# Kernel tuning notes

Hardware: AMD Instinct MI355X
Metric: run time of the kernel (lower is better)

The kernel has to match this reference:

```python
import jax, jax.numpy as jnp
import numpy as np

N_QUBITS = 12
RANK = 1024
K = 4            # outcomes per qubit
D = 2 ** N_QUBITS
N_IDX = 1_000_000


def setup_inputs() -> dict:
    key = jax.random.key(0)
    k1, k2, k3, k4 = jax.random.split(key, 4)
    params = jax.random.normal(k1, (2, D, RANK), dtype=jnp.float32)
    M_real = jax.random.normal(k2, (K, 2, 2), dtype=jnp.float32)
    M_imag = jax.random.normal(k3, (K, 2, 2), dtype=jnp.float32)
    P_idxs = jax.random.randint(k4, (N_IDX,), 0, K ** N_QUBITS, dtype=jnp.int64)
    return {"params": params, "M_real": M_real, "M_imag": M_imag, "P_idxs": P_idxs}


def _qmt(rho, M, n_qubits):
    """Born rule: P[s1..sN] = Tr[(M_{s1} x ... x M_{sN}) rho].
    Sequential per-qubit contraction; T has shape [K^n, 2^(N-n), 2^(N-n)]."""
    T = rho[None, :, :]  # axes: (done outcomes, row legs j, col legs i)
    for _ in range(n_qubits):
        k, r, c = T.shape[0], T.shape[1] // 2, T.shape[2] // 2
        Tt = T.reshape(k, 2, r, 2, c)  # (k, j_n, j_rest, i_n, i_rest)
        # Tr contribution: sum_{i,j} M[s,i,j] * rho[j,i]
        T = jnp.einsum('sij,kjait->ksat', M, Tt).reshape(k * M.shape[0], r, c)
    return T.reshape(-1)  # [K^N] complex


def reference(params, M_real, M_imag, P_idxs):
    # rho = U U^H / Tr(U U^H)
    U = jax.lax.complex(params[0], params[1])            # [D, RANK] complex64
    rho = U @ U.conj().T                                  # [D, D]
    rho = rho / jnp.trace(rho)
    M = jax.lax.complex(M_real, M_imag)                   # [K, 2, 2] complex64
    P_all = _qmt(rho, M, N_QUBITS).real                   # [K^N] float32
    return P_all[P_idxs]
```

## Files before the change

kernel.cpp:

```cpp
#include <hip/hip_runtime.h>

#define D 4096
#define RANK 1024
#define K2 2048
#define UELEMS 4194304ULL
#define NTOT 16777216ULL
#define QSCALE 16000.0f

typedef __attribute__((ext_vector_type(4))) int i32x4;

__device__ float g_inv_tr[1];
__device__ float g_scale[D];
__device__ float g_mdre[16];
__device__ float g_mdim[16];

static __device__ __forceinline__ void load_lds16(const void* g, void* l) {
    __builtin_amdgcn_global_load_lds(
        (const __attribute__((address_space(1))) unsigned int*)g,
        (__attribute__((address_space(3))) unsigned int*)l, 16, 0, 0);
}

__global__ __launch_bounds__(256) void convert_w_i8(const float* __restrict__ P,
                                                    const float* __restrict__ Mre,
                                                    const float* __restrict__ Mim,
                                                    char* __restrict__ Wh,
                                                    char* __restrict__ Wl,
                                                    char* __restrict__ N2h,
                                                    char* __restrict__ N2l)
{
    if (blockIdx.x == 0 && threadIdx.x < 16) {
        const int s = threadIdx.x >> 2, i = (threadIdx.x >> 1) & 1, j = threadIdx.x & 1;
        g_mdre[threadIdx.x] =  Mre[s * 4 + j * 2 + i];
        g_mdim[threadIdx.x] = -Mim[s * 4 + j * 2 + i];
    }

    const int w = threadIdx.x >> 6, lane = threadIdx.x & 63;
    const int row = blockIdx.x * 4 + w;

    float ur[16], ui[16];
    const float* pr = P + (size_t)row * RANK + lane * 16;
    const float* pi = P + UELEMS + (size_t)row * RANK + lane * 16;
    #pragma unroll
    for (int q = 0; q < 4; ++q) {
        const float4 a = ((const float4*)pr)[q];
        const float4 b = ((const float4*)pi)[q];
        ur[q * 4 + 0] = a.x; ur[q * 4 + 1] = a.y; ur[q * 4 + 2] = a.z; ur[q * 4 + 3] = a.w;
        ui[q * 4 + 0] = b.x; ui[q * 4 + 1] = b.y; ui[q * 4 + 2] = b.z; ui[q * 4 + 3] = b.w;
    }
    float mx = 0.f;
    #pragma unroll
    for (int e = 0; e < 16; ++e)
        mx = fmaxf(mx, fmaxf(fabsf(ur[e]), fabsf(ui[e])));
    #pragma unroll
    for (int off = 1; off < 64; off <<= 1)
        mx = fmaxf(mx, __shfl_xor(mx, off));
    const float inv = mx > 0.f ? QSCALE / mx : 0.f;
    if (lane == 0) g_scale[row] = mx / QSCALE;

    int hr[16], lr[16], hi[16], li[16];
    #pragma unroll
    for (int e = 0; e < 16; ++e) {
        float q = ur[e] * inv;
        float hf = rintf(q * 0.0078125f);
        hr[e] = (int)hf; lr[e] = (int)rintf(q - 128.f * hf);
        q = ui[e] * inv;
        hf = rintf(q * 0.0078125f);
        hi[e] = (int)hf; li[e] = (int)rintf(q - 128.f * hf);
    }
    uint4 phr, plr, phi, pli, pnh, pnl;
    unsigned* dst[6] = {(unsigned*)&phr, (unsigned*)&plr, (unsigned*)&phi,
                        (unsigned*)&pli, (unsigned*)&pnh, (unsigned*)&pnl};
    #pragma unroll
    for (int q = 0; q < 4; ++q) {
        unsigned a = 0, b = 0, c = 0, d = 0, e = 0, f = 0;
        #pragma unroll
        for (int k = 0; k < 4; ++k) {
            const int sh = k * 8;
            a |= (unsigned)(hr[q * 4 + k] & 255) << sh;
            b |= (unsigned)(lr[q * 4 + k] & 255) << sh;
            c |= (unsigned)(hi[q * 4 + k] & 255) << sh;
            d |= (unsigned)(li[q * 4 + k] & 255) << sh;
            e |= (unsigned)((-hi[q * 4 + k]) & 255) << sh;
            f |= (unsigned)((-li[q * 4 + k]) & 255) << sh;
        }
        dst[0][q] = a; dst[1][q] = b; dst[2][q] = c; dst[3][q] = d; dst[4][q] = e; dst[5][q] = f;
    }
    const size_t b1 = (size_t)row * 2048 + lane * 16;
    *(uint4*)&Wh[b1] = phr;          *(uint4*)&Wl[b1] = plr;
    *(uint4*)&Wh[b1 + 1024] = phi;   *(uint4*)&Wl[b1 + 1024] = pli;
    const size_t b2 = (size_t)row * 1024 + lane * 16;
    *(uint4*)&N2h[b2] = pnh;         *(uint4*)&N2l[b2] = pnl;
}

__global__ __launch_bounds__(256, 2) void gemm_rho_i8(const char* __restrict__ Wh,
                                                      const char* __restrict__ Wl,
                                                      const char* __restrict__ N2h,
                                                      const char* __restrict__ N2l,
                                                      float2* __restrict__ rho)
{
    __shared__ __align__(16) char sA1h[64 * 64];
    __shared__ __align__(16) char sA1l[64 * 64];
    __shared__ __align__(16) char sA2h[64 * 64];
    __shared__ __align__(16) char sA2l[64 * 64];
    __shared__ __align__(16) char sB1h[128 * 64];
    __shared__ __align__(16) char sB1l[128 * 64];
    __shared__ __align__(16) char sB2h[128 * 64];
    __shared__ __align__(16) char sB2l[128 * 64];
    __shared__ __align__(16) char sN2h[128 * 64];
    __shared__ __align__(16) char sN2l[128 * 64];

    const int b = blockIdx.x;
    int bj = (int)((65.0f - sqrtf(4225.0f - 4.0f * (float)b)) * 0.5f);
    while (bj > 0 && bj * (65 - bj) > b) --bj;
    while ((bj + 1) * (64 - bj) <= b) ++bj;
    const int bi = 2 * bj + (b - bj * (65 - bj));
    const int row0 = bi << 6, col0 = bj << 7;
    const bool full = (bi >= 2 * bj + 2);

    const int t = threadIdx.x;
    const int lane = t & 63, w = t >> 6;
    const int wr = w >> 1, wc = w & 1;

    const int rowA = t >> 2;
    const int kcA = (t & 3) ^ ((rowA >> 1) & 3);
    const size_t aoff = (size_t)(row0 + rowA) * 2048 + kcA * 16;
    const int ldsA = t * 16;
    size_t boff[2], boffN[2]; int ldsB[2];
    #pragma unroll
    for (int q = 0; q < 2; ++q) {
        const int g = q * 256 + t;
        const int rowB = g >> 2;
        const int kcB = (g & 3) ^ ((rowB >> 1) & 3);
        boff[q]  = (size_t)(col0 + rowB) * 2048 + kcB * 16;
        boffN[q] = (size_t)(col0 + rowB) * 1024 + kcB * 16;
        ldsB[q] = g * 16;
    }

    const int m = lane & 15, gq = lane >> 4;
    const int fko = (gq ^ ((m >> 1) & 3)) * 16;

    i32x4 rehh[2][4], remx[2][4], imhh[2][4], immx[2][4];
    #pragma unroll
    for (int i = 0; i < 2; ++i)
        #pragma unroll
        for (int j = 0; j < 4; ++j) {
            rehh[i][j] = (i32x4){0, 0, 0, 0}; remx[i][j] = (i32x4){0, 0, 0, 0};
            imhh[i][j] = (i32x4){0, 0, 0, 0}; immx[i][j] = (i32x4){0, 0, 0, 0};
        }

    for (int kt = 0; kt < RANK; kt += 64) {
        load_lds16(Wh + aoff + kt,        &sA1h[ldsA]);
        load_lds16(Wl + aoff + kt,        &sA1l[ldsA]);
        load_lds16(Wh + aoff + kt + 1024, &sA2h[ldsA]);
        load_lds16(Wl + aoff + kt + 1024, &sA2l[ldsA]);
        #pragma unroll
        for (int q = 0; q < 2; ++q) {
            load_lds16(Wh + boff[q] + kt,        &sB1h[ldsB[q]]);
            load_lds16(Wl + boff[q] + kt,        &sB1l[ldsB[q]]);
            load_lds16(Wh + boff[q] + kt + 1024, &sB2h[ldsB[q]]);
            load_lds16(Wl + boff[q] + kt + 1024, &sB2l[ldsB[q]]);
            load_lds16(N2h + boffN[q] + kt,      &sN2h[ldsB[q]]);
            load_lds16(N2l + boffN[q] + kt,      &sN2l[ldsB[q]]);
        }
        __syncthreads();

        i32x4 fa1h[2], fa1l[2], fa2h[2], fa2l[2];
        #pragma unroll
        for (int i = 0; i < 2; ++i) {
            const int off = (wr * 32 + i * 16 + m) * 64 + fko;
            fa1h[i] = *(const i32x4*)&sA1h[off];
            fa1l[i] = *(const i32x4*)&sA1l[off];
            fa2h[i] = *(const i32x4*)&sA2h[off];
            fa2l[i] = *(const i32x4*)&sA2l[off];
        }
        #pragma unroll
        for (int j = 0; j < 4; ++j) {
            const int off = (wc * 64 + j * 16 + m) * 64 + fko;
            const i32x4 b1h = *(const i32x4*)&sB1h[off];
            const i32x4 b1l = *(const i32x4*)&sB1l[off];
            const i32x4 b2h = *(const i32x4*)&sB2h[off];
            const i32x4 b2l = *(const i32x4*)&sB2l[off];
            const i32x4 n2h = *(const i32x4*)&sN2h[off];
            const i32x4 n2l = *(const i32x4*)&sN2l[off];
            #pragma unroll
            for (int i = 0; i < 2; ++i) {
                i32x4 r = rehh[i][j];
                r = __builtin_amdgcn_mfma_i32_16x16x64_i8(fa1h[i], b1h, r, 0, 0, 0);
                r = __builtin_amdgcn_mfma_i32_16x16x64_i8(fa2h[i], b2h, r, 0, 0, 0);
                rehh[i][j] = r;
                r = remx[i][j];
                r = __builtin_amdgcn_mfma_i32_16x16x64_i8(fa1h[i], b1l, r, 0, 0, 0);
                r = __builtin_amdgcn_mfma_i32_16x16x64_i8(fa1l[i], b1h, r, 0, 0, 0);
                r = __builtin_amdgcn_mfma_i32_16x16x64_i8(fa2h[i], b2l, r, 0, 0, 0);
                r = __builtin_amdgcn_mfma_i32_16x16x64_i8(fa2l[i], b2h, r, 0, 0, 0);
                remx[i][j] = r;
                r = imhh[i][j];
                r = __builtin_amdgcn_mfma_i32_16x16x64_i8(fa2h[i], b1h, r, 0, 0, 0);
                r = __builtin_amdgcn_mfma_i32_16x16x64_i8(fa1h[i], n2h, r, 0, 0, 0);
                imhh[i][j] = r;
                r = immx[i][j];
                r = __builtin_amdgcn_mfma_i32_16x16x64_i8(fa2h[i], b1l, r, 0, 0, 0);
                r = __builtin_amdgcn_mfma_i32_16x16x64_i8(fa2l[i], b1h, r, 0, 0, 0);
                r = __builtin_amdgcn_mfma_i32_16x16x64_i8(fa1h[i], n2l, r, 0, 0, 0);
                r = __builtin_amdgcn_mfma_i32_16x16x64_i8(fa1l[i], n2h, r, 0, 0, 0);
                immx[i][j] = r;
            }
        }
        __syncthreads();
    }

    #pragma unroll
    for (int i = 0; i < 2; ++i)
        #pragma unroll
        for (int j = 0; j < 4; ++j) {
            const int col = col0 + wc * 64 + j * 16 + m;
            const float sc = g_scale[col];
            #pragma unroll
            for (int r = 0; r < 4; ++r) {
                const int row = row0 + wr * 32 + i * 16 + gq * 4 + r;
                const float s2 = g_scale[row] * sc;
                const float re = s2 * (16384.f * (float)rehh[i][j][r] + 128.f * (float)remx[i][j][r]);
                const float im = s2 * (16384.f * (float)imhh[i][j][r] + 128.f * (float)immx[i][j][r]);
                if (full || row >= col) rho[(size_t)row * D + col] = make_float2(re, im);
                if (row > col && ((row >> 6) == (col >> 6)))
                    rho[(size_t)col * D + row] = make_float2(re, -im);
            }
        }
}

__global__ void trace_inv(const float2* __restrict__ rho)
{
    __shared__ float red[256];
    float s = 0.f;
    for (int d = threadIdx.x; d < D; d += 256)
        s += rho[(size_t)d * (D + 1)].x;
    red[threadIdx.x] = s;
    __syncthreads();
    for (int off = 128; off > 0; off >>= 1) {
        if (threadIdx.x < off) red[threadIdx.x] += red[threadIdx.x + off];
        __syncthreads();
    }
    if (threadIdx.x == 0) g_inv_tr[0] = 1.0f / red[0];
}

static __device__ __forceinline__ void qmt2(float2* x,
                                            const float* __restrict__ Mre,
                                            const float* __restrict__ Mim)
{
    float2 y[16];
    #pragma unroll
    for (int sb = 0; sb < 4; ++sb)
        #pragma unroll
        for (int ja = 0; ja < 2; ++ja)
            #pragma unroll
            for (int ia = 0; ia < 2; ++ia) {
                float2 acc = make_float2(0.f, 0.f);
                #pragma unroll
                for (int ib = 0; ib < 2; ++ib)
                    #pragma unroll
                    for (int jb = 0; jb < 2; ++jb) {
                        const float mr = Mre[sb * 4 + ib * 2 + jb];
                        const float mi = Mim[sb * 4 + ib * 2 + jb];
                        const float2 v = x[(ja * 2 + jb) * 4 + ia * 2 + ib];
                        acc.x += mr * v.x - mi * v.y;
                        acc.y += mr * v.y + mi * v.x;
                    }
                y[sb * 4 + ja * 2 + ia] = acc;
            }
    #pragma unroll
    for (int sa = 0; sa < 4; ++sa)
        #pragma unroll
        for (int sb = 0; sb < 4; ++sb) {
            float2 acc = make_float2(0.f, 0.f);
            #pragma unroll
            for (int ia = 0; ia < 2; ++ia)
                #pragma unroll
                for (int ja = 0; ja < 2; ++ja) {
                    const float mr = Mre[sa * 4 + ia * 2 + ja];
                    const float mi = Mim[sa * 4 + ia * 2 + ja];
                    const float2 v = y[sb * 4 + ja * 2 + ia];
                    acc.x += mr * v.x - mi * v.y;
                    acc.y += mr * v.y + mi * v.x;
                }
            x[sa * 4 + sb] = acc;
        }
}

static __device__ __forceinline__ void pA_pipeline(float2* x, float2* X, const int t,
                                                   const float* __restrict__ mre,
                                                   const float* __restrict__ mim)
{
    qmt2(x, mre, mim);
    #pragma unroll
    for (int d = 0; d < 16; ++d) X[t * 17 + d] = x[d];
    __syncthreads();
    const int a2 = t >> 6, t2 = (t >> 4) & 3, d1 = t & 15;
    #pragma unroll
    for (int j2 = 0; j2 < 4; ++j2)
        #pragma unroll
        for (int i2 = 0; i2 < 4; ++i2)
            x[j2 * 4 + i2] = X[((a2 * 4 + j2) * 16 + t2 * 4 + i2) * 17 + d1];
    __syncthreads();
    qmt2(x, mre, mim);
    #pragma unroll
    for (int d = 0; d < 16; ++d) X[(a2 * 4 + t2) * 257 + d * 16 + d1] = x[d];
    __syncthreads();
    const int e2 = t >> 4, e1 = t & 15;
    #pragma unroll
    for (int j2 = 0; j2 < 4; ++j2)
        #pragma unroll
        for (int i2 = 0; i2 < 4; ++i2)
            x[j2 * 4 + i2] = X[(j2 * 4 + i2) * 257 + e2 * 16 + e1];
    qmt2(x, mre, mim);
}

__global__ __launch_bounds__(256) void qmt_pAh(const float2* __restrict__ in,
                                               float2* __restrict__ out,
                                               const float* __restrict__ Mre,
                                               const float* __restrict__ Mim)
{
    __shared__ __align__(16) float2 X[256 * 17];
    const int t = threadIdx.x;
    const int g = blockIdx.x;
    int rr = (int)((sqrtf(8.f * (float)g + 1.f) - 1.f) * 0.5f);
    while (rr * (rr + 1) / 2 > g) --rr;
    while ((rr + 1) * (rr + 2) / 2 <= g) ++rr;
    const int cc = g - rr * (rr + 1) / 2;

    const int a4 = t >> 4, t4 = t & 15;
    float2 x0[16], x[16];
    #pragma unroll
    for (int j2 = 0; j2 < 4; ++j2) {
        const float2* p = in + ((size_t)(rr * 64 + a4 * 4 + j2)) * 4096 + cc * 64 + t4 * 4;
        const float4 v0 = ((const float4*)p)[0];
        const float4 v1 = ((const float4*)p)[1];
        x0[j2 * 4 + 0] = make_float2(v0.x, v0.y);
        x0[j2 * 4 + 1] = make_float2(v0.z, v0.w);
        x0[j2 * 4 + 2] = make_float2(v1.x, v1.y);
        x0[j2 * 4 + 3] = make_float2(v1.z, v1.w);
    }

    #pragma unroll
    for (int q = 0; q < 16; ++q) x[q] = x0[q];
    pA_pipeline(x, X, t, Mre, Mim);
    const int e2 = t >> 4, e1 = t & 15;
    const size_t ob0 = (size_t)(rr * 64 + cc) * 4096 + e2 * 16 + e1;
    #pragma unroll
    for (int d = 0; d < 16; ++d) out[ob0 + (size_t)d * 256] = x[d];

    if (rr != cc) {
        __syncthreads();
        #pragma unroll
        for (int q = 0; q < 16; ++q) x[q] = x0[q];
        pA_pipeline(x, X, t, g_mdre, g_mdim);
        const size_t ob1 = (size_t)(cc * 64 + rr) * 4096 + e2 * 16 + e1;
        #pragma unroll
        for (int d = 0; d < 16; ++d)
            out[ob1 + (size_t)d * 256] = make_float2(x[d].x, -x[d].y);
    }
}

static __device__ __forceinline__ void qmt_stage_cb(float2* x,
                                                    const float* __restrict__ Mre,
                                                    const float* __restrict__ Mim)
{
    #pragma unroll
    for (int jj = 0; jj < 4; ++jj) {
        float2 y[16];
        #pragma unroll
        for (int sc = 0; sc < 4; ++sc)
            #pragma unroll
            for (int ii = 0; ii < 4; ++ii) {
                float2 acc = make_float2(0.f, 0.f);
                #pragma unroll
                for (int ic = 0; ic < 2; ++ic)
                    #pragma unroll
                    for (int jc = 0; jc < 2; ++jc) {
                        const float mr = Mre[sc * 4 + ic * 2 + jc];
                        const float mi = Mim[sc * 4 + ic * 2 + jc];
                        const float2 v = x[jj * 16 + jc * 8 + ii * 2 + ic];
                        acc.x += mr * v.x - mi * v.y;
                        acc.y += mr * v.y + mi * v.x;
                    }
                y[sc * 4 + ii] = acc;
            }
        #pragma unroll
        for (int q = 0; q < 16; ++q) x[jj * 16 + q] = y[q];
    }

    #pragma unroll
    for (int ja = 0; ja < 2; ++ja)
        #pragma unroll
        for (int sc = 0; sc < 4; ++sc) {
            float2 z[8];
            #pragma unroll
            for (int sb = 0; sb < 4; ++sb)
                #pragma unroll
                for (int ia = 0; ia < 2; ++ia) {
                    float2 acc = make_float2(0.f, 0.f);
                    #pragma unroll
                    for (int ib = 0; ib < 2; ++ib)
                        #pragma unroll
                        for (int jb = 0; jb < 2; ++jb) {
                            const float mr = Mre[sb * 4 + ib * 2 + jb];
                            const float mi = Mim[sb * 4 + ib * 2 + jb];
                            const float2 v = x[(ja * 2 + jb) * 16 + sc * 4 + ia * 2 + ib];
                            acc.x += mr * v.x - mi * v.y;
                            acc.y += mr * v.y + mi * v.x;
                        }
                    z[sb * 2 + ia] = acc;
                }
            #pragma unroll
            for (int sb = 0; sb < 4; ++sb)
                #pragma unroll
                for (int ia = 0; ia < 2; ++ia)
                    x[ja * 32 + (sb >> 1) * 16 + sc * 4 + ia * 2 + (sb & 1)] = z[sb * 2 + ia];
        }
}

#define QMT_STAGE_A(STORE)                                                     \
    _Pragma("unroll")                                                          \
    for (int sbH = 0; sbH < 2; ++sbH)                                          \
        _Pragma("unroll")                                                      \
        for (int sc = 0; sc < 4; ++sc)                                         \
            _Pragma("unroll")                                                  \
            for (int sbL = 0; sbL < 2; ++sbL) {                                \
                const int sb = sbH * 2 + sbL;                                  \
                _Pragma("unroll")                                              \
                for (int sa = 0; sa < 4; ++sa) {                               \
                    float2 acc = make_float2(0.f, 0.f);                        \
                    _Pragma("unroll")                                          \
                    for (int ia = 0; ia < 2; ++ia)                             \
                        _Pragma("unroll")                                      \
                        for (int ja = 0; ja < 2; ++ja) {                       \
                            const float mr = Mre[sa * 4 + ia * 2 + ja];        \
                            const float mi = Mim[sa * 4 + ia * 2 + ja];        \
                            const float2 v = x[ja * 32 + sbH * 16 + sc * 4 + ia * 2 + sbL]; \
                            acc.x += mr * v.x - mi * v.y;                      \
                            acc.y += mr * v.y + mi * v.x;                      \
                        }                                                      \
                    const int s3 = sa * 16 + sb * 4 + sc;                      \
                    STORE;                                                     \
                }                                                              \
            }

__global__ __launch_bounds__(256) void qmt_p3(const float2* __restrict__ in,
                                              float2* __restrict__ out,
                                              const float* __restrict__ Mre,
                                              const float* __restrict__ Mim)
{
    const int tid = blockIdx.x * 256 + threadIdx.x;
    const int s = tid & 4095, c3 = (tid >> 12) & 7, r3 = tid >> 15;

    float2 x[64];
    #pragma unroll
    for (int j3 = 0; j3 < 8; ++j3)
        #pragma unroll
        for (int i3 = 0; i3 < 8; ++i3)
            x[j3 * 8 + i3] = in[(size_t)((r3 * 8 + j3) * 64 + c3 * 8 + i3) * 4096 + s];
    qmt_stage_cb(x, Mre, Mim);
    const size_t ob = ((size_t)(r3 * 8 + c3) * 64) * 4096 + s;
    QMT_STAGE_A(out[ob + s3 * 4096] = acc)
}

__global__ __launch_bounds__(256) void qmt_p4(const float2* __restrict__ in,
                                              float* __restrict__ out,
                                              const float* __restrict__ Mre,
                                              const float* __restrict__ Mim)
{
    const int tid = blockIdx.x * 256 + threadIdx.x;
    float2 x[64];
    #pragma unroll
    for (int j3 = 0; j3 < 8; ++j3)
        #pragma unroll
        for (int i3 = 0; i3 < 8; ++i3)
            x[j3 * 8 + i3] = in[(size_t)(j3 * 8 + i3) * 262144 + tid];
    qmt_stage_cb(x, Mre, Mim);
    const size_t ob = (size_t)(tid >> 5) * 2048 + (tid & 31);
    QMT_STAGE_A(out[ob + s3 * 32] = acc.x)
}

__global__ void gather_idx(const float* __restrict__ P, const int* __restrict__ idxs,
                           float* __restrict__ out, const int n)
{
    const int i = blockIdx.x * 256 + threadIdx.x;
    if (i < n) {
        const int idx = idxs[i];
        const int s = idx & 262143;
        const size_t pos = (size_t)(s >> 5) * 2048 + (size_t)(idx >> 18) * 32 + (s & 31);
        out[i] = P[pos] * g_inv_tr[0];
    }
}

extern "C" void kernel_launch(void* const* d_in, const int* in_sizes, int n_in,
                              void* d_out, int out_size, void* d_ws, size_t ws_size,
                              hipStream_t stream)
{
    const float* params = (const float*)d_in[0];
    const float* Mre    = (const float*)d_in[1];
    const float* Mim    = (const float*)d_in[2];
    const int*   idxs   = (const int*)d_in[3];
    float*       out    = (float*)d_out;

    float* ws = (float*)d_ws;
    float2* A  = (float2*)ws;
    float2* Bp = (float2*)(ws + 2 * NTOT);
    char* Wh  = (char*)Bp;
    char* Wl  = Wh + (size_t)D * 2048;
    char* N2h = Wl + (size_t)D * 2048;
    char* N2l = N2h + (size_t)D * 1024;

    convert_w_i8<<<1024, 256, 0, stream>>>(params, Mre, Mim, Wh, Wl, N2h, N2l);
    gemm_rho_i8<<<1056, 256, 0, stream>>>(Wh, Wl, N2h, N2l, A);
    trace_inv<<<1, 256, 0, stream>>>(A);

    qmt_pAh<<<2080, 256, 0, stream>>>(A, Bp, Mre, Mim);
    qmt_p3<<<1024, 256, 0, stream>>>(Bp, A, Mre, Mim);
    qmt_p4<<<1024, 256, 0, stream>>>(A, (float*)Bp, Mre, Mim);

    gather_idx<<<(out_size + 255) / 256, 256, 0, stream>>>((float*)Bp, idxs, out, out_size);
}
```

Measured before the change: 431.8 us.

## Double-buffer int8 rho GEMM, drop negated-imag operand, retile to 128x64 blocks

Rewrites the split-int8 MFMA GEMM that forms rho = U U^H. It drops the precomputed negated-imaginary operands (N2h/N2l) and instead keeps separate accumulators for the two cross terms, subtracting them in the epilogue. The kernel moves to 512 threads with 128x64 tiles and double-buffered LDS, so global-to-LDS loads for the next K-step overlap with MFMA work. It also adds s_setprio and sched barriers around the MFMA blocks. This removes converter writes and GEMM operand loads, at the cost of more accumulator registers, more barriers, and a different lower-triangular tile mapping.

```diff
diff --git a/kernel.cpp b/kernel.cpp
--- a/kernel.cpp
+++ b/kernel.cpp
@@ -2,7 +2,6 @@
 
 #define D 4096
 #define RANK 1024
-#define K2 2048
 #define UELEMS 4194304ULL
 #define NTOT 16777216ULL
 #define QSCALE 16000.0f
@@ -20,13 +19,13 @@
         (__attribute__((address_space(3))) unsigned int*)l, 16, 0, 0);
 }
 
+#define MFMA_I8 __builtin_amdgcn_mfma_i32_16x16x64_i8
+
 __global__ __launch_bounds__(256) void convert_w_i8(const float* __restrict__ P,
                                                     const float* __restrict__ Mre,
                                                     const float* __restrict__ Mim,
                                                     char* __restrict__ Wh,
-                                                    char* __restrict__ Wl,
-                                                    char* __restrict__ N2h,
-                                                    char* __restrict__ N2l)
+                                                    char* __restrict__ Wl)
 {
     if (blockIdx.x == 0 && threadIdx.x < 16) {
         const int s = threadIdx.x >> 2, i = (threadIdx.x >> 1) & 1, j = threadIdx.x & 1;
@@ -67,12 +66,11 @@
         hf = rintf(q * 0.0078125f);
         hi[e] = (int)hf; li[e] = (int)rintf(q - 128.f * hf);
     }
-    uint4 phr, plr, phi, pli, pnh, pnl;
-    unsigned* dst[6] = {(unsigned*)&phr, (unsigned*)&plr, (unsigned*)&phi,
-                        (unsigned*)&pli, (unsigned*)&pnh, (unsigned*)&pnl};
+    uint4 phr, plr, phi, pli;
+    unsigned* dst[4] = {(unsigned*)&phr, (unsigned*)&plr, (unsigned*)&phi, (unsigned*)&pli};
     #pragma unroll
     for (int q = 0; q < 4; ++q) {
-        unsigned a = 0, b = 0, c = 0, d = 0, e = 0, f = 0;
+        unsigned a = 0, b = 0, c = 0, d = 0;
         #pragma unroll
         for (int k = 0; k < 4; ++k) {
             const int sh = k * 8;
@@ -80,152 +78,177 @@
             b |= (unsigned)(lr[q * 4 + k] & 255) << sh;
             c |= (unsigned)(hi[q * 4 + k] & 255) << sh;
             d |= (unsigned)(li[q * 4 + k] & 255) << sh;
-            e |= (unsigned)((-hi[q * 4 + k]) & 255) << sh;
-            f |= (unsigned)((-li[q * 4 + k]) & 255) << sh;
-        }
-        dst[0][q] = a; dst[1][q] = b; dst[2][q] = c; dst[3][q] = d; dst[4][q] = e; dst[5][q] = f;
+        }
+        dst[0][q] = a; dst[1][q] = b; dst[2][q] = c; dst[3][q] = d;
     }
     const size_t b1 = (size_t)row * 2048 + lane * 16;
     *(uint4*)&Wh[b1] = phr;          *(uint4*)&Wl[b1] = plr;
     *(uint4*)&Wh[b1 + 1024] = phi;   *(uint4*)&Wl[b1 + 1024] = pli;
-    const size_t b2 = (size_t)row * 1024 + lane * 16;
-    *(uint4*)&N2h[b2] = pnh;         *(uint4*)&N2l[b2] = pnl;
-}
-
-__global__ __launch_bounds__(256, 2) void gemm_rho_i8(const char* __restrict__ Wh,
+}
+
+__global__ __launch_bounds__(512, 2) void gemm_rho_i8(const char* __restrict__ Wh,
                                                       const char* __restrict__ Wl,
-                                                      const char* __restrict__ N2h,
-                                                      const char* __restrict__ N2l,
                                                       float2* __restrict__ rho)
 {
-    __shared__ __align__(16) char sA1h[64 * 64];
-    __shared__ __align__(16) char sA1l[64 * 64];
-    __shared__ __align__(16) char sA2h[64 * 64];
-    __shared__ __align__(16) char sA2l[64 * 64];
-    __shared__ __align__(16) char sB1h[128 * 64];
-    __shared__ __align__(16) char sB1l[128 * 64];
-    __shared__ __align__(16) char sB2h[128 * 64];
-    __shared__ __align__(16) char sB2l[128 * 64];
-    __shared__ __align__(16) char sN2h[128 * 64];
-    __shared__ __align__(16) char sN2l[128 * 64];
-
-    const int b = blockIdx.x;
-    int bj = (int)((65.0f - sqrtf(4225.0f - 4.0f * (float)b)) * 0.5f);
-    while (bj > 0 && bj * (65 - bj) > b) --bj;
-    while ((bj + 1) * (64 - bj) <= b) ++bj;
-    const int bi = 2 * bj + (b - bj * (65 - bj));
-    const int row0 = bi << 6, col0 = bj << 7;
-    const bool full = (bi >= 2 * bj + 2);
+    __shared__ __align__(16) char sA[2][4][128 * 64];
+    __shared__ __align__(16) char sB[2][4][64 * 64];
+
+    const int g = blockIdx.x;
+    int bi = (int)((sqrtf(4.f * (float)g + 1.f) - 1.f) * 0.5f);
+    while (bi > 0 && bi * (bi + 1) > g) --bi;
+    while ((bi + 1) * (bi + 2) <= g) ++bi;
+    const int bj = g - bi * (bi + 1);
+    const int row0 = bi << 7, col0 = bj << 6;
 
     const int t = threadIdx.x;
     const int lane = t & 63, w = t >> 6;
     const int wr = w >> 1, wc = w & 1;
 
-    const int rowA = t >> 2;
-    const int kcA = (t & 3) ^ ((rowA >> 1) & 3);
-    const size_t aoff = (size_t)(row0 + rowA) * 2048 + kcA * 16;
-    const int ldsA = t * 16;
-    size_t boff[2], boffN[2]; int ldsB[2];
-    #pragma unroll
-    for (int q = 0; q < 2; ++q) {
-        const int g = q * 256 + t;
-        const int rowB = g >> 2;
-        const int kcB = (g & 3) ^ ((rowB >> 1) & 3);
-        boff[q]  = (size_t)(col0 + rowB) * 2048 + kcB * 16;
-        boffN[q] = (size_t)(col0 + rowB) * 1024 + kcB * 16;
-        ldsB[q] = g * 16;
-    }
+    const int ra = t >> 2;
+    const int kca = (t & 3) ^ ((ra >> 1) & 3);
+    const size_t aoff = (size_t)(row0 + ra) * 2048 + kca * 16;
+    const int ldsAo = t * 16;
+    const int tb = t & 255;
+    const int rb = tb >> 2;
+    const int kcb = (t & 3) ^ ((rb >> 1) & 3);
+    const int hiw = (t >= 256) ? 1 : 0;
+    const size_t boff = (size_t)(col0 + rb) * 2048 + kcb * 16 + hiw * 1024;
+    const int ldsB0o = hiw * 8192 + tb * 16;
+    const int ldsB1o = ldsB0o + 4096;
 
     const int m = lane & 15, gq = lane >> 4;
     const int fko = (gq ^ ((m >> 1) & 3)) * 16;
 
-    i32x4 rehh[2][4], remx[2][4], imhh[2][4], immx[2][4];
+    i32x4 rehh[2][2], remx[2][2], iphh[2][2], ipmx[2][2], iqhh[2][2], iqmx[2][2];
     #pragma unroll
     for (int i = 0; i < 2; ++i)
         #pragma unroll
-        for (int j = 0; j < 4; ++j) {
+        for (int j = 0; j < 2; ++j) {
             rehh[i][j] = (i32x4){0, 0, 0, 0}; remx[i][j] = (i32x4){0, 0, 0, 0};
-            imhh[i][j] = (i32x4){0, 0, 0, 0}; immx[i][j] = (i32x4){0, 0, 0, 0};
-        }
-
-    for (int kt = 0; kt < RANK; kt += 64) {
-        load_lds16(Wh + aoff + kt,        &sA1h[ldsA]);
-        load_lds16(Wl + aoff + kt,        &sA1l[ldsA]);
-        load_lds16(Wh + aoff + kt + 1024, &sA2h[ldsA]);
-        load_lds16(Wl + aoff + kt + 1024, &sA2l[ldsA]);
-        #pragma unroll
-        for (int q = 0; q < 2; ++q) {
-            load_lds16(Wh + boff[q] + kt,        &sB1h[ldsB[q]]);
-            load_lds16(Wl + boff[q] + kt,        &sB1l[ldsB[q]]);
-            load_lds16(Wh + boff[q] + kt + 1024, &sB2h[ldsB[q]]);
-            load_lds16(Wl + boff[q] + kt + 1024, &sB2l[ldsB[q]]);
-            load_lds16(N2h + boffN[q] + kt,      &sN2h[ldsB[q]]);
-            load_lds16(N2l + boffN[q] + kt,      &sN2l[ldsB[q]]);
-        }
-        __syncthreads();
+            iphh[i][j] = (i32x4){0, 0, 0, 0}; ipmx[i][j] = (i32x4){0, 0, 0, 0};
+            iqhh[i][j] = (i32x4){0, 0, 0, 0}; iqmx[i][j] = (i32x4){0, 0, 0, 0};
+        }
+
+    char* const sA0 = &sA[0][0][0];
+    char* const sB0 = &sB[0][0][0];
+
+    load_lds16(Wh + aoff,        sA0 + ldsAo);
+    load_lds16(Wl + aoff,        sA0 + 8192  + ldsAo);
+    load_lds16(Wh + aoff + 1024, sA0 + 16384 + ldsAo);
+    load_lds16(Wl + aoff + 1024, sA0 + 24576 + ldsAo);
+    load_lds16(Wh + boff,        sB0 + ldsB0o);
+    load_lds16(Wl + boff,        sB0 + ldsB1o);
+    __syncthreads();
+
+#define DO_MFMA_J(j)                                                          \
+    _Pragma("unroll")                                                         \
+    for (int i = 0; i < 2; ++i) {                                             \
+        i32x4 r;                                                              \
+        r = rehh[i][j];                                                       \
+        r = MFMA_I8(fa1h[i], b1h, r, 0, 0, 0);                                \
+        r = MFMA_I8(fa2h[i], b2h, r, 0, 0, 0);                                \
+        rehh[i][j] = r;                                                       \
+        r = remx[i][j];                                                       \
+        r = MFMA_I8(fa1h[i], b1l, r, 0, 0, 0);                                \
+        r = MFMA_I8(fa1l[i], b1h, r, 0, 0, 0);                                \
+        r = MFMA_I8(fa2h[i], b2l, r, 0, 0, 0);                                \
+        r = MFMA_I8(fa2l[i], b2h, r, 0, 0, 0);                                \
+        remx[i][j] = r;                                                       \
+        r = MFMA_I8(fa2h[i], b1h, iphh[i][j], 0, 0, 0); iphh[i][j] = r;       \
+        r = ipmx[i][j];                                                       \
+        r = MFMA_I8(fa2h[i], b1l, r, 0, 0, 0);                                \
+        r = MFMA_I8(fa2l[i], b1h, r, 0, 0, 0);                                \
+        ipmx[i][j] = r;                                                       \
+        r = MFMA_I8(fa1h[i], b2h, iqhh[i][j], 0, 0, 0); iqhh[i][j] = r;       \
+        r = iqmx[i][j];                                                       \
+        r = MFMA_I8(fa1h[i], b2l, r, 0, 0, 0);                                \
+        r = MFMA_I8(fa1l[i], b2h, r, 0, 0, 0);                                \
+        iqmx[i][j] = r;                                                       \
+    }
+
+    #pragma unroll 2
+    for (int kt = 0; kt < 16; ++kt) {
+        const int cur = kt & 1;
+        const char* sAc = sA0 + cur * 32768;
+        const char* sBc = sB0 + cur * 16384;
+        char* sAn = sA0 + (cur ^ 1) * 32768;
+        char* sBn = sB0 + (cur ^ 1) * 16384;
+        const size_t ko = (size_t)(kt + 1) * 64;
 
         i32x4 fa1h[2], fa1l[2], fa2h[2], fa2l[2];
+        i32x4 b1h, b1l, b2h, b2l;
+
         #pragma unroll
         for (int i = 0; i < 2; ++i) {
             const int off = (wr * 32 + i * 16 + m) * 64 + fko;
-            fa1h[i] = *(const i32x4*)&sA1h[off];
-            fa1l[i] = *(const i32x4*)&sA1l[off];
-            fa2h[i] = *(const i32x4*)&sA2h[off];
-            fa2l[i] = *(const i32x4*)&sA2l[off];
-        }
-        #pragma unroll
-        for (int j = 0; j < 4; ++j) {
-            const int off = (wc * 64 + j * 16 + m) * 64 + fko;
-            const i32x4 b1h = *(const i32x4*)&sB1h[off];
-            const i32x4 b1l = *(const i32x4*)&sB1l[off];
-            const i32x4 b2h = *(const i32x4*)&sB2h[off];
-            const i32x4 b2l = *(const i32x4*)&sB2l[off];
-            const i32x4 n2h = *(const i32x4*)&sN2h[off];
-            const i32x4 n2l = *(const i32x4*)&sN2l[off];
-            #pragma unroll
-            for (int i = 0; i < 2; ++i) {
-                i32x4 r = rehh[i][j];
-                r = __builtin_amdgcn_mfma_i32_16x16x64_i8(fa1h[i], b1h, r, 0, 0, 0);
-                r = __builtin_amdgcn_mfma_i32_16x16x64_i8(fa2h[i], b2h, r, 0, 0, 0);
-                rehh[i][j] = r;
-                r = remx[i][j];
-                r = __builtin_amdgcn_mfma_i32_16x16x64_i8(fa1h[i], b1l, r, 0, 0, 0);
-                r = __builtin_amdgcn_mfma_i32_16x16x64_i8(fa1l[i], b1h, r, 0, 0, 0);
-                r = __builtin_amdgcn_mfma_i32_16x16x64_i8(fa2h[i], b2l, r, 0, 0, 0);
-                r = __builtin_amdgcn_mfma_i32_16x16x64_i8(fa2l[i], b2h, r, 0, 0, 0);
-                remx[i][j] = r;
-                r = imhh[i][j];
-                r = __builtin_amdgcn_mfma_i32_16x16x64_i8(fa2h[i], b1h, r, 0, 0, 0);
-                r = __builtin_amdgcn_mfma_i32_16x16x64_i8(fa1h[i], n2h, r, 0, 0, 0);
-                imhh[i][j] = r;
-                r = immx[i][j];
-                r = __builtin_amdgcn_mfma_i32_16x16x64_i8(fa2h[i], b1l, r, 0, 0, 0);
-                r = __builtin_amdgcn_mfma_i32_16x16x64_i8(fa2l[i], b1h, r, 0, 0, 0);
-                r = __builtin_amdgcn_mfma_i32_16x16x64_i8(fa1h[i], n2l, r, 0, 0, 0);
-                r = __builtin_amdgcn_mfma_i32_16x16x64_i8(fa1l[i], n2h, r, 0, 0, 0);
-                immx[i][j] = r;
-            }
-        }
+            fa1h[i] = *(const i32x4*)(sAc + off);
+            fa1l[i] = *(const i32x4*)(sAc + 8192  + off);
+            fa2h[i] = *(const i32x4*)(sAc + 16384 + off);
+            fa2l[i] = *(const i32x4*)(sAc + 24576 + off);
+        }
+        {
+            const int off = (wc * 32 + m) * 64 + fko;
+            b1h = *(const i32x4*)(sBc + off);
+            b1l = *(const i32x4*)(sBc + 4096  + off);
+            b2h = *(const i32x4*)(sBc + 8192  + off);
+            b2l = *(const i32x4*)(sBc + 12288 + off);
+        }
+        if (kt < 15) {
+            load_lds16(Wh + aoff + ko,        sAn + ldsAo);
+            load_lds16(Wl + aoff + ko,        sAn + 8192  + ldsAo);
+            load_lds16(Wh + aoff + ko + 1024, sAn + 16384 + ldsAo);
+            load_lds16(Wl + aoff + ko + 1024, sAn + 24576 + ldsAo);
+        }
+        __builtin_amdgcn_s_barrier();
+        asm volatile("s_waitcnt lgkmcnt(0)" ::: "memory");
+        __builtin_amdgcn_sched_barrier(0);
+        __builtin_amdgcn_s_setprio(1);
+        DO_MFMA_J(0)
+        __builtin_amdgcn_s_setprio(0);
+        __builtin_amdgcn_s_barrier();
+
+        {
+            const int off = (wc * 32 + 16 + m) * 64 + fko;
+            b1h = *(const i32x4*)(sBc + off);
+            b1l = *(const i32x4*)(sBc + 4096  + off);
+            b2h = *(const i32x4*)(sBc + 8192  + off);
+            b2l = *(const i32x4*)(sBc + 12288 + off);
+        }
+        if (kt < 15) {
+            load_lds16(Wh + boff + ko, sBn + ldsB0o);
+            load_lds16(Wl + boff + ko, sBn + ldsB1o);
+        }
+        __builtin_amdgcn_s_barrier();
+        asm volatile("s_waitcnt lgkmcnt(0)" ::: "memory");
+        __builtin_amdgcn_sched_barrier(0);
+        __builtin_amdgcn_s_setprio(1);
+        DO_MFMA_J(1)
+        __builtin_amdgcn_s_setprio(0);
+
         __syncthreads();
     }
-
-    #pragma unroll
-    for (int i = 0; i < 2; ++i)
-        #pragma unroll
-        for (int j = 0; j < 4; ++j) {
-            const int col = col0 + wc * 64 + j * 16 + m;
-            const float sc = g_scale[col];
+#undef DO_MFMA_J
+
+    #pragma unroll
+    for (int j = 0; j < 2; ++j) {
+        const int col = col0 + wc * 32 + j * 16 + m;
+        const float sc = g_scale[col];
+        const int c64 = col >> 6;
+        #pragma unroll
+        for (int i = 0; i < 2; ++i) {
             #pragma unroll
             for (int r = 0; r < 4; ++r) {
                 const int row = row0 + wr * 32 + i * 16 + gq * 4 + r;
                 const float s2 = g_scale[row] * sc;
                 const float re = s2 * (16384.f * (float)rehh[i][j][r] + 128.f * (float)remx[i][j][r]);
-                const float im = s2 * (16384.f * (float)imhh[i][j][r] + 128.f * (float)immx[i][j][r]);
-                if (full || row >= col) rho[(size_t)row * D + col] = make_float2(re, im);
-                if (row > col && ((row >> 6) == (col >> 6)))
-                    rho[(size_t)col * D + row] = make_float2(re, -im);
+                const float im = s2 * (16384.f * (float)(iphh[i][j][r] - iqhh[i][j][r])
+                                      + 128.f * (float)(ipmx[i][j][r] - iqmx[i][j][r]));
+                const int r64 = row >> 6;
+                if (r64 > c64 || row >= col) rho[(size_t)row * D + col] = make_float2(re, im);
+                if (r64 == c64 && row > col) rho[(size_t)col * D + row] = make_float2(re, -im);
             }
         }
+    }
 }
 
 __global__ void trace_inv(const float2* __restrict__ rho)
@@ -505,13 +528,11 @@
     float* ws = (float*)d_ws;
     float2* A  = (float2*)ws;
     float2* Bp = (float2*)(ws + 2 * NTOT);
-    char* Wh  = (char*)Bp;
-    char* Wl  = Wh + (size_t)D * 2048;
-    char* N2h = Wl + (size_t)D * 2048;
-    char* N2l = N2h + (size_t)D * 1024;
-
-    convert_w_i8<<<1024, 256, 0, stream>>>(params, Mre, Mim, Wh, Wl, N2h, N2l);
-    gemm_rho_i8<<<1056, 256, 0, stream>>>(Wh, Wl, N2h, N2l, A);
+    char* Wh = (char*)Bp;
+    char* Wl = Wh + (size_t)D * 2048;
+
+    convert_w_i8<<<1024, 256, 0, stream>>>(params, Mre, Mim, Wh, Wl);
+    gemm_rho_i8<<<1056, 512, 0, stream>>>(Wh, Wl, A);
     trace_inv<<<1, 256, 0, stream>>>(A);
 
     qmt_pAh<<<2080, 256, 0, stream>>>(A, Bp, Mre, Mim);
```

Result: slower. 601.0 us (+39.2%).
